# Performance work log

Measured on AMD Instinct MI355X. Metric: run time of the kernel, lower is better.

The kernel has to match this reference:

```python
import jax, jax.numpy as jnp
import numpy as np

TEMPERATURE = 0.2
EPS = 1e-12

def _l2norm(v, axis=-1):
    return v / jnp.maximum(jnp.linalg.norm(v, axis=axis, keepdims=True), EPS)

def setup_inputs() -> dict:
    key = jax.random.key(0)
    k1, k2, k3, k4, k5 = jax.random.split(key, 5)
    B, D, P, K = 4096, 256, 100, 10
    return {
        "x": jax.random.normal(k1, (B, D), dtype=jnp.float32),
        "x_aug": jax.random.normal(k2, (B, D), dtype=jnp.float32),
        "proto_w": jax.random.normal(k3, (P, D), dtype=jnp.float32),
        "hard_q": jax.random.randint(k4, (2, B), 0, P, dtype=jnp.int32),
        "neg_q": jax.random.randint(k5, (2, B, K), 0, P, dtype=jnp.int32),
    }

def reference(x, x_aug, proto_w, hard_q, neg_q):
    # graphcl.loss_cal with args.hard_selection=True, args.proto_dist=True,
    # args.sample_dist=False. The original O(n^2) python loops are vectorized
    # as gathers/broadcasts; math is identical.
    B = x.shape[0]
    P = proto_w.shape[0]
    out1 = _l2norm(x)                      # [B, D]
    out2 = _l2norm(x_aug)                  # [B, D]
    out = jnp.concatenate([out1, out2], 0) # [2B, D]
    n = 2 * B

    sim = jnp.exp(out @ out.T / TEMPERATURE)          # [2B, 2B]
    eye = jnp.eye(n, dtype=bool)

    hq = hard_q.reshape(-1)                # [2B]  (concat of the two views)
    nq = neg_q.reshape(n, -1)              # [2B, K]

    # hard_selection: mask[i,j] = (i != j) and (hard_q[j] in neg_q[i]).
    # Build per-prototype membership [2B, P], then gather columns by hq[j].
    mem_proto = (nq[:, :, None] == jnp.arange(P, dtype=nq.dtype)[None, None, :]).any(1)  # [2B, P]
    member = jnp.take(mem_proto, hq, axis=1)          # [2B, 2B]
    mask = (~eye) & member

    # proto_dist reweighting (prototypes used via .data, i.e. detached).
    w = _l2norm(jax.lax.stop_gradient(proto_w))       # [P, D]
    pd = 1.0 - w @ w.T                                # [P, P]
    rw = jnp.where(eye, 0.0, pd[hq[:, None], hq[None, :]])  # [2B, 2B]
    rmin = rw.min(axis=1, keepdims=True)
    rmax = rw.max(axis=1, keepdims=True)
    rw = (rw - rmin) / (rmax - rmin)
    # NOTE: torch broadcasts (2B,2B) - (2B,) along columns -> mu[None, :]
    mu = rw.mean(axis=1)
    std = jnp.std(rw, axis=1, ddof=1)  # torch.std default: unbiased
    rw = jnp.exp((rw - mu[None, :]) ** 2 / (2.0 * std[None, :] ** 2))
    sim = sim * rw

    pos = jnp.exp(jnp.sum(out1 * out2, axis=-1) / TEMPERATURE)  # [B]
    pos = jnp.concatenate([pos, pos], 0)                        # [2B]
    # masked_select(...).sum(dim=-1) in the original sums ALL kept entries.
    denom = jnp.sum(jnp.where(mask, sim, 0.0))
    loss = jnp.mean(-jnp.log(pos / denom))
    return loss
```

## Files before the change

### kernel.cpp

```cpp
#include <hip/hip_runtime.h>
#include <cmath>

#define BB   4096
#define DD   256
#define NN   8192
#define PP   100
#define KK   10

typedef float f32x16 __attribute__((ext_vector_type(16)));
typedef long  lx2    __attribute__((ext_vector_type(2)));

constexpr size_t OFF_DPART = 0;
constexpr size_t OFF_PPART = 4096;
constexpr size_t OFF_CNT   = 8192;
constexpr size_t OFF_MU    = 8704;
constexpr size_t OFF_SD    = 9216;
constexpr size_t OFF_RWN   = 9728;
constexpr size_t OFF_BASE  = 49728;
constexpr size_t OFF_PI    = 56128;
constexpr size_t OFF_INVP  = 88896;
constexpr size_t OFF_HQP   = 121664;
constexpr size_t OFF_CTABT = 154432;
constexpr size_t OFF_G     = 3431232;


__global__ __launch_bounds__(1024) void prep_kernel(
    const int* __restrict__ hq, int* __restrict__ cnt, int* __restrict__ base16,
    double* __restrict__ dpart, double* __restrict__ ppart) {
    __shared__ int h[16][PP];
    __shared__ int sc[PP];
    const int t = threadIdx.x;
    h[t & 15][t >> 4] = 0;
    if (t < 576) h[(t + 1024) & 15][(t + 1024) >> 4] = 0;
    if (t < 512) dpart[t] = 0.0; else ppart[t - 512] = 0.0;
    __syncthreads();
#pragma unroll
    for (int r = 0; r < 8; ++r) {
        const int i = r * 1024 + t;
        atomicAdd(&h[2 * r + (t >> 9)][hq[i]], 1);
    }
    __syncthreads();
    int bb[16];
    if (t < PP) {
        int s = 0;
#pragma unroll
        for (int ch = 0; ch < 16; ++ch) { bb[ch] = s; s += h[ch][t]; }
        cnt[t] = s;
        sc[t] = s;
    }
    __syncthreads();
    if (t == 0) {
        int run = 0;
        for (int c = 0; c < PP; ++c) { int v = sc[c]; sc[c] = run; run += v; }
    }
    __syncthreads();
    if (t < PP) {
        const int cb = sc[t];
#pragma unroll
        for (int ch = 0; ch < 16; ++ch) base16[ch * PP + t] = cb + bb[ch];
    }
}

__global__ __launch_bounds__(256) void scatter_kernel(
    const int* __restrict__ hq, const int* __restrict__ base16,
    int* __restrict__ pi, int* __restrict__ invp, int* __restrict__ hqp) {
    __shared__ int cur[PP];
    const int t = threadIdx.x;
    const int ch = blockIdx.x;
    if (t < PP) cur[t] = base16[ch * PP + t];
    __syncthreads();
#pragma unroll
    for (int r = 0; r < 2; ++r) {
        const int i = ch * 512 + r * 256 + t;
        const int c = hq[i];
        const int d = atomicAdd(&cur[c], 1);
        pi[d] = i;
        hqp[d] = c;
        invp[i] = d;
    }
}

__global__ __launch_bounds__(256) void norm_protopd_kernel(
    const float* __restrict__ x, const float* __restrict__ xa,
    const float* __restrict__ pw, const int* __restrict__ invp,
    const int* __restrict__ cnt, char* __restrict__ Gpb, double* __restrict__ ppart,
    float* __restrict__ rwn, float* __restrict__ mu, float* __restrict__ sd) {
    const int blk = blockIdx.x;
    const int t = threadIdx.x;
    if (blk < 1024) {
        const int wv = t >> 6, lane = t & 63;
        const int i = blk * 4 + wv;
        const float4 v1 = *(const float4*)(x  + (size_t)i * DD + lane * 4);
        const float4 v2 = *(const float4*)(xa + (size_t)i * DD + lane * 4);
        float a = v1.x * v1.x + v1.y * v1.y + v1.z * v1.z + v1.w * v1.w;
        float b = v2.x * v2.x + v2.y * v2.y + v2.z * v2.z + v2.w * v2.w;
        float c = v1.x * v2.x + v1.y * v2.y + v1.z * v2.z + v1.w * v2.w;
#pragma unroll
        for (int off = 32; off > 0; off >>= 1) {
            a += __shfl_xor(a, off);
            b += __shfl_xor(b, off);
            c += __shfl_xor(c, off);
        }
        const float d1 = fmaxf(sqrtf(a), 1e-12f), i1 = 1.0f / d1;
        const float d2 = fmaxf(sqrtf(b), 1e-12f), i2 = 1.0f / d2;
        const int p1 = invp[i];
        const int p2 = invp[i + BB];
        int w1 = __builtin_amdgcn_cvt_pk_fp8_f32(v1.x * i1, v1.y * i1, 0, false);
        w1 = __builtin_amdgcn_cvt_pk_fp8_f32(v1.z * i1, v1.w * i1, w1, true);
        int w2 = __builtin_amdgcn_cvt_pk_fp8_f32(v2.x * i2, v2.y * i2, 0, false);
        w2 = __builtin_amdgcn_cvt_pk_fp8_f32(v2.z * i2, v2.w * i2, w2, true);
        const int q = lane >> 3, halfsel = (lane >> 1) & 1, pairsel = (lane >> 2) & 1;
        const int bo = pairsel * 8 + 4 * (lane & 1);
        const size_t a1 = (size_t)((p1 >> 5) * 8192 + q * 1024 +
                                   (halfsel * 32 + (p1 & 31)) * 16 + bo);
        const size_t a2 = (size_t)((p2 >> 5) * 8192 + q * 1024 +
                                   (halfsel * 32 + (p2 & 31)) * 16 + bo);
        *(int*)(Gpb + a1) = w1;
        *(int*)(Gpb + a2) = w2;
        if (lane == 0) atomicAdd(&ppart[i & 511], (double)(c * i1 * i2));
    } else {
        const int a = blk - 1024;
        __shared__ alignas(16) float wa[DD];
        __shared__ float pdrow[PP];
        __shared__ float r4[4];
        float av = pw[(size_t)a * DD + t];
        float ss = av * av;
#pragma unroll
        for (int off = 32; off > 0; off >>= 1) ss += __shfl_down(ss, off);
        if ((t & 63) == 0) r4[t >> 6] = ss;
        __syncthreads();
        const float na = fmaxf(sqrtf(r4[0] + r4[1] + r4[2] + r4[3]), 1e-12f);
        wa[t] = av / na;
        __syncthreads();
        if (t < PP) {
            const float4* wc = (const float4*)(pw + (size_t)t * DD);
            float dot = 0.f, nb = 0.f;
#pragma unroll 4
            for (int k = 0; k < 64; ++k) {
                const float4 w = wc[k];
                const float4 u = *(const float4*)(wa + 4 * k);
                dot += u.x * w.x + u.y * w.y + u.z * w.z + u.w * w.w;
                nb += w.x * w.x + w.y * w.y + w.z * w.z + w.w * w.w;
            }
            pdrow[t] = 1.0f - dot / fmaxf(sqrtf(nb), 1e-12f);
        }
        __syncthreads();
        if (t < 64) {
            const int lane = t;
            float vmin = 0.f, vmax = 0.f;
            for (int b = lane; b < PP; b += 64) {
                int cc = cnt[b] - (b == a ? 1 : 0);
                if (cc > 0) {
                    float v = pdrow[b];
                    vmin = fminf(vmin, v);
                    vmax = fmaxf(vmax, v);
                }
            }
#pragma unroll
            for (int off = 32; off > 0; off >>= 1) {
                vmin = fminf(vmin, __shfl_xor(vmin, off));
                vmax = fmaxf(vmax, __shfl_xor(vmax, off));
            }
            const float den = vmax - vmin;
            const float inv = (den > 0.f) ? 1.f / den : 0.f;
            double s1 = 0.0, s2 = 0.0;
            for (int b = lane; b < PP; b += 64) {
                float v = (pdrow[b] - vmin) * inv;
                rwn[a * PP + b] = v;
                int cc = cnt[b] - (b == a ? 1 : 0);
                if (cc > 0) { double dv = v; s1 += cc * dv; s2 += cc * dv * dv; }
            }
            if (lane == 0) { double v0 = (0.0 - (double)vmin) * inv; s1 += v0; s2 += v0 * v0; }
#pragma unroll
            for (int off = 32; off > 0; off >>= 1) {
                s1 += __shfl_xor(s1, off);
                s2 += __shfl_xor(s2, off);
            }
            if (lane == 0) {
                double m = s1 / (double)NN;
                double var = (s2 - (double)NN * m * m) / (double)(NN - 1);
                mu[a] = (float)m;
                sd[a] = (float)sqrt(fmax(var, 0.0));
            }
        }
    }
}

__global__ __launch_bounds__(256) void ctab_kernel(
    const int* __restrict__ pi, const int* __restrict__ hqp, const int* __restrict__ nq,
    const float* __restrict__ rwn, const float* __restrict__ mu, const float* __restrict__ sd,
    float* __restrict__ CtabT) {
    const int p0 = blockIdx.x * 32;
    const int t = threadIdx.x;
    __shared__ unsigned long long bits[32][2];
    __shared__ int cls[32];
    __shared__ float smu[PP], ssd[PP];
    if (t < 32) {
        const int p = p0 + t;
        const int* row = nq + (size_t)pi[p] * KK;
        unsigned long long b0 = 0, b1 = 0;
#pragma unroll
        for (int k = 0; k < KK; ++k) {
            int c = row[k];
            if (c < 64) b0 |= 1ull << c; else b1 |= 1ull << (c - 64);
        }
        bits[t][0] = b0;
        bits[t][1] = b1;
        cls[t] = hqp[p];
    }
    if (t < PP) { smu[t] = mu[t]; ssd[t] = sd[t]; }
    __syncthreads();
    for (int idx = t; idx < 32 * PP; idx += 256) {
        const int c = idx >> 5;
        const int pl = idx & 31;
        const bool m = (c < 64) ? ((bits[pl][0] >> c) & 1) : ((bits[pl][1] >> (c - 64)) & 1);
        float v = 0.f;
        if (m) {
            float d = rwn[cls[pl] * PP + c] - smu[c];
            float s = ssd[c];
            v = expf(d * d / (2.0f * s * s));
        }
        CtabT[(size_t)c * NN + p0 + pl] = v;
    }
}

__device__ __forceinline__ void gload_lds16(void* g, void* l) {
    typedef __attribute__((address_space(1))) void* as1_void_p;
    typedef __attribute__((address_space(3))) void* as3_void_p;
    __builtin_amdgcn_global_load_lds((as1_void_p)g, (as3_void_p)l, 16, 0, 0);
}

__global__ __launch_bounds__(256) void sim_kernel(
    const char* __restrict__ Gpb, const int* __restrict__ hqp,
    const float* __restrict__ CtabT, double* __restrict__ dpart) {
    const int xcd = blockIdx.x & 7;
    int idx0 = blockIdx.x >> 3;
    if (idx0 >= 496 + (xcd >> 1) * 16) return;
    int idx = idx0;
    int bj = 0, bi = 0;
#pragma unroll
    for (int q = 0; q < 16; ++q) {
        const int bjq = xcd + 8 * q;
        const int c = (bjq >> 1) + 1;
        if (idx < c) { bj = bjq; bi = idx; break; }
        idx -= c;
    }

    const int t = threadIdx.x;
    const int lane = t & 63;
    const int wv = t >> 6;
    const int i0w = bi * 128 + wv * 32;
    const int j0 = bj * 64;

    __shared__ alignas(16) char lB[16384];

    const char* pa = Gpb + (size_t)(i0w >> 5) * 8192 + lane * 16;
    lx2 a[8];
#pragma unroll
    for (int q = 0; q < 8; ++q) a[q] = *(const lx2*)(pa + q * 1024);

    char* gB = const_cast<char*>(Gpb) + (size_t)(j0 >> 5) * 8192;
#pragma unroll
    for (int s = 0; s < 4; ++s) {
        const int off = (s * 4 + wv) * 1024;
        gload_lds16(gB + off + lane * 16, lB + off);
    }

    const int cl = lane & 31, h = lane >> 5;
    const int col0 = j0 + cl;
    const int col1 = j0 + 32 + cl;
    const int cls0 = hqp[col0];
    const int cls1 = hqp[col1];
    int4 rcg[4];
#pragma unroll
    for (int g = 0; g < 4; ++g)
        rcg[g] = *(const int4*)(hqp + i0w + 8 * g + 4 * h);

    __syncthreads();

    f32x16 acc[2] = {};
#pragma unroll
    for (int q = 0; q < 8; ++q) {
        const lx2 b0 = *(const lx2*)(lB + q * 1024 + lane * 16);
        const lx2 b1 = *(const lx2*)(lB + 8192 + q * 1024 + lane * 16);
        acc[0] = __builtin_amdgcn_mfma_f32_32x32x16_fp8_fp8(a[q].x, b0.x, acc[0], 0, 0, 0);
        acc[1] = __builtin_amdgcn_mfma_f32_32x32x16_fp8_fp8(a[q].x, b1.x, acc[1], 0, 0, 0);
        acc[0] = __builtin_amdgcn_mfma_f32_32x32x16_fp8_fp8(a[q].y, b0.y, acc[0], 0, 0, 0);
        acc[1] = __builtin_amdgcn_mfma_f32_32x32x16_fp8_fp8(a[q].y, b1.y, acc[1], 0, 0, 0);
    }

    const float* ct0 = CtabT + (size_t)cls0 * NN;
    const float* ct1 = CtabT + (size_t)cls1 * NN;
    float partial = 0.f;
#pragma unroll
    for (int g = 0; g < 4; ++g) {
        const int rbase = i0w + 8 * g + 4 * h;
        const float4 cf0 = *(const float4*)(ct0 + rbase);
        const float4 cf1 = *(const float4*)(ct1 + rbase);
        const float* f0 = (const float*)&cf0;
        const float* f1 = (const float*)&cf1;
        const int rcv[4] = {rcg[g].x, rcg[g].y, rcg[g].z, rcg[g].w};
#pragma unroll
        for (int r = 0; r < 4; ++r) {
            const int row = rbase + r;
            const float* ctr = CtabT + (size_t)rcv[r] * NN;
            const float c20 = ctr[col0];
            const float c21 = ctr[col1];
            const float e0 = __expf(acc[0][4 * g + r] * 5.0f);
            const float e1 = __expf(acc[1][4 * g + r] * 5.0f);
            partial += (row < col0) ? e0 * (f0[r] + c20) : 0.f;
            partial += (row < col1) ? e1 * (f1[r] + c21) : 0.f;
        }
    }
#pragma unroll
    for (int off = 32; off > 0; off >>= 1) partial += __shfl_down(partial, off);
    __shared__ float wsum[4];
    if (lane == 0) wsum[wv] = partial;
    __syncthreads();
    if (t == 0) {
        const int slot = (xcd * 8 + (idx0 & 7)) * 8 + ((idx0 >> 3) & 7);
        atomicAdd(&dpart[slot], (double)(wsum[0] + wsum[1] + wsum[2] + wsum[3]));
    }
}

__global__ void finalize_kernel(const double* __restrict__ dpart,
                                const double* __restrict__ ppart, float* __restrict__ out) {
    const int lane = threadIdx.x;
    double d = 0.0, p = 0.0;
#pragma unroll
    for (int k = 0; k < 8; ++k) {
        d += dpart[lane + 64 * k];
        p += ppart[lane + 64 * k];
    }
#pragma unroll
    for (int off = 32; off > 0; off >>= 1) {
        d += __shfl_down(d, off);
        p += __shfl_down(p, off);
    }
    if (lane == 0) out[0] = (float)(log(d) - p * (5.0 / 4096.0));
}

extern "C" void kernel_launch(void* const* d_in, const int* in_sizes, int n_in,
                              void* d_out, int out_size, void* d_ws, size_t ws_size,
                              hipStream_t stream) {
    const float* x  = (const float*)d_in[0];
    const float* xa = (const float*)d_in[1];
    const float* pw = (const float*)d_in[2];
    const int* hq   = (const int*)d_in[3];
    const int* nq   = (const int*)d_in[4];
    float* out      = (float*)d_out;

    char* ws = (char*)d_ws;
    double* dpart = (double*)(ws + OFF_DPART);
    double* ppart = (double*)(ws + OFF_PPART);
    int* cnt      = (int*)(ws + OFF_CNT);
    float* mu     = (float*)(ws + OFF_MU);
    float* sd     = (float*)(ws + OFF_SD);
    float* rwn    = (float*)(ws + OFF_RWN);
    int* base16   = (int*)(ws + OFF_BASE);
    int* pi       = (int*)(ws + OFF_PI);
    int* invp     = (int*)(ws + OFF_INVP);
    int* hqp      = (int*)(ws + OFF_HQP);
    float* CtabT  = (float*)(ws + OFF_CTABT);
    char* Gpb     = (char*)(ws + OFF_G);

    prep_kernel<<<1, 1024, 0, stream>>>(hq, cnt, base16, dpart, ppart);
    scatter_kernel<<<16, 256, 0, stream>>>(hq, base16, pi, invp, hqp);
    norm_protopd_kernel<<<1124, 256, 0, stream>>>(x, xa, pw, invp, cnt, Gpb, ppart,
                                                  rwn, mu, sd);
    ctab_kernel<<<NN / 32, 256, 0, stream>>>(pi, hqp, nq, rwn, mu, sd, CtabT);
    sim_kernel<<<8 * 544, 256, 0, stream>>>(Gpb, hqp, CtabT, dpart);
    finalize_kernel<<<1, 64, 0, stream>>>(dpart, ppart, out);
}
```

Measured before the change: 125.9 us.

## Merge prep and scatter kernels, batch norm rows per wave, hoist Ctab loads

Folds the single-block histogram/prefix kernel and the 16-block scatter kernel into one 17-block kernel. Each block recomputes the full histogram redundantly to get its own scatter bases, and an extra block zeroes the accumulators and writes the class counts. The normalization kernel now handles four rows per wave with loads issued up front, which cuts its block count and the number of ppart atomics. In the sim kernel, all Ctab gathers are issued before the exp/accumulate loop to overlap their latency. The cost is redundant histogram work per block and higher register pressure.

```diff
diff --git a/kernel.cpp b/kernel.cpp
--- a/kernel.cpp
+++ b/kernel.cpp
@@ -16,7 +16,6 @@
 constexpr size_t OFF_MU    = 8704;
 constexpr size_t OFF_SD    = 9216;
 constexpr size_t OFF_RWN   = 9728;
-constexpr size_t OFF_BASE  = 49728;
 constexpr size_t OFF_PI    = 56128;
 constexpr size_t OFF_INVP  = 88896;
 constexpr size_t OFF_HQP   = 121664;
@@ -24,56 +23,59 @@
 constexpr size_t OFF_G     = 3431232;
 
 
-__global__ __launch_bounds__(1024) void prep_kernel(
-    const int* __restrict__ hq, int* __restrict__ cnt, int* __restrict__ base16,
+__global__ __launch_bounds__(256) void sortzero_kernel(
+    const int* __restrict__ hq, int* __restrict__ cnt,
+    int* __restrict__ pi, int* __restrict__ invp, int* __restrict__ hqp,
     double* __restrict__ dpart, double* __restrict__ ppart) {
+    const int blk = blockIdx.x;
+    const int t = threadIdx.x;
+    if (blk == 16) {
+        for (int k = t; k < 512; k += 256) { dpart[k] = 0.0; ppart[k] = 0.0; }
+        __shared__ int hh[PP];
+        if (t < PP) hh[t] = 0;
+        __syncthreads();
+#pragma unroll
+        for (int r = 0; r < 32; ++r) atomicAdd(&hh[hq[r * 256 + t]], 1);
+        __syncthreads();
+        if (t < PP) cnt[t] = hh[t];
+        return;
+    }
     __shared__ int h[16][PP];
-    __shared__ int sc[PP];
-    const int t = threadIdx.x;
-    h[t & 15][t >> 4] = 0;
-    if (t < 576) h[(t + 1024) & 15][(t + 1024) >> 4] = 0;
-    if (t < 512) dpart[t] = 0.0; else ppart[t - 512] = 0.0;
-    __syncthreads();
-#pragma unroll
-    for (int r = 0; r < 8; ++r) {
-        const int i = r * 1024 + t;
-        atomicAdd(&h[2 * r + (t >> 9)][hq[i]], 1);
-    }
-    __syncthreads();
-    int bb[16];
+    __shared__ int tot[PP];
+    __shared__ int gbase[PP];
+    __shared__ int base[PP];
+    int* hf = &h[0][0];
+    for (int k = t; k < 16 * PP; k += 256) hf[k] = 0;
+    __syncthreads();
+#pragma unroll
+    for (int r = 0; r < 32; ++r) {
+        const int i = r * 256 + t;
+        atomicAdd(&h[r >> 1][hq[i]], 1);
+    }
+    __syncthreads();
     if (t < PP) {
-        int s = 0;
-#pragma unroll
-        for (int ch = 0; ch < 16; ++ch) { bb[ch] = s; s += h[ch][t]; }
-        cnt[t] = s;
-        sc[t] = s;
+        int pre = 0, s = 0;
+#pragma unroll
+        for (int ch = 0; ch < 16; ++ch) {
+            if (ch == blk) pre = s;
+            s += h[ch][t];
+        }
+        tot[t] = s;
+        base[t] = pre;
     }
     __syncthreads();
     if (t == 0) {
         int run = 0;
-        for (int c = 0; c < PP; ++c) { int v = sc[c]; sc[c] = run; run += v; }
-    }
-    __syncthreads();
-    if (t < PP) {
-        const int cb = sc[t];
-#pragma unroll
-        for (int ch = 0; ch < 16; ++ch) base16[ch * PP + t] = cb + bb[ch];
-    }
-}
-
-__global__ __launch_bounds__(256) void scatter_kernel(
-    const int* __restrict__ hq, const int* __restrict__ base16,
-    int* __restrict__ pi, int* __restrict__ invp, int* __restrict__ hqp) {
-    __shared__ int cur[PP];
-    const int t = threadIdx.x;
-    const int ch = blockIdx.x;
-    if (t < PP) cur[t] = base16[ch * PP + t];
+        for (int c = 0; c < PP; ++c) { gbase[c] = run; run += tot[c]; }
+    }
+    __syncthreads();
+    if (t < PP) base[t] += gbase[t];
     __syncthreads();
 #pragma unroll
     for (int r = 0; r < 2; ++r) {
-        const int i = ch * 512 + r * 256 + t;
+        const int i = blk * 512 + r * 256 + t;
         const int c = hq[i];
-        const int d = atomicAdd(&cur[c], 1);
+        const int d = atomicAdd(&base[c], 1);
         pi[d] = i;
         hqp[d] = c;
         invp[i] = d;
@@ -87,39 +89,50 @@
     float* __restrict__ rwn, float* __restrict__ mu, float* __restrict__ sd) {
     const int blk = blockIdx.x;
     const int t = threadIdx.x;
-    if (blk < 1024) {
+    if (blk < 256) {
         const int wv = t >> 6, lane = t & 63;
-        const int i = blk * 4 + wv;
-        const float4 v1 = *(const float4*)(x  + (size_t)i * DD + lane * 4);
-        const float4 v2 = *(const float4*)(xa + (size_t)i * DD + lane * 4);
-        float a = v1.x * v1.x + v1.y * v1.y + v1.z * v1.z + v1.w * v1.w;
-        float b = v2.x * v2.x + v2.y * v2.y + v2.z * v2.z + v2.w * v2.w;
-        float c = v1.x * v2.x + v1.y * v2.y + v1.z * v2.z + v1.w * v2.w;
-#pragma unroll
-        for (int off = 32; off > 0; off >>= 1) {
-            a += __shfl_xor(a, off);
-            b += __shfl_xor(b, off);
-            c += __shfl_xor(c, off);
-        }
-        const float d1 = fmaxf(sqrtf(a), 1e-12f), i1 = 1.0f / d1;
-        const float d2 = fmaxf(sqrtf(b), 1e-12f), i2 = 1.0f / d2;
-        const int p1 = invp[i];
-        const int p2 = invp[i + BB];
-        int w1 = __builtin_amdgcn_cvt_pk_fp8_f32(v1.x * i1, v1.y * i1, 0, false);
-        w1 = __builtin_amdgcn_cvt_pk_fp8_f32(v1.z * i1, v1.w * i1, w1, true);
-        int w2 = __builtin_amdgcn_cvt_pk_fp8_f32(v2.x * i2, v2.y * i2, 0, false);
-        w2 = __builtin_amdgcn_cvt_pk_fp8_f32(v2.z * i2, v2.w * i2, w2, true);
+        const int w = blk * 4 + wv;
+        float4 v1[4], v2[4];
+        int p1[4], p2[4];
+#pragma unroll
+        for (int s = 0; s < 4; ++s) {
+            const int i = w + 1024 * s;
+            v1[s] = *(const float4*)(x  + (size_t)i * DD + lane * 4);
+            v2[s] = *(const float4*)(xa + (size_t)i * DD + lane * 4);
+            p1[s] = invp[i];
+            p2[s] = invp[i + BB];
+        }
         const int q = lane >> 3, halfsel = (lane >> 1) & 1, pairsel = (lane >> 2) & 1;
         const int bo = pairsel * 8 + 4 * (lane & 1);
-        const size_t a1 = (size_t)((p1 >> 5) * 8192 + q * 1024 +
-                                   (halfsel * 32 + (p1 & 31)) * 16 + bo);
-        const size_t a2 = (size_t)((p2 >> 5) * 8192 + q * 1024 +
-                                   (halfsel * 32 + (p2 & 31)) * 16 + bo);
-        *(int*)(Gpb + a1) = w1;
-        *(int*)(Gpb + a2) = w2;
-        if (lane == 0) atomicAdd(&ppart[i & 511], (double)(c * i1 * i2));
+        double psum = 0.0;
+#pragma unroll
+        for (int s = 0; s < 4; ++s) {
+            float a = v1[s].x * v1[s].x + v1[s].y * v1[s].y + v1[s].z * v1[s].z + v1[s].w * v1[s].w;
+            float b = v2[s].x * v2[s].x + v2[s].y * v2[s].y + v2[s].z * v2[s].z + v2[s].w * v2[s].w;
+            float c = v1[s].x * v2[s].x + v1[s].y * v2[s].y + v1[s].z * v2[s].z + v1[s].w * v2[s].w;
+#pragma unroll
+            for (int off = 32; off > 0; off >>= 1) {
+                a += __shfl_xor(a, off);
+                b += __shfl_xor(b, off);
+                c += __shfl_xor(c, off);
+            }
+            const float d1 = fmaxf(sqrtf(a), 1e-12f), i1 = 1.0f / d1;
+            const float d2 = fmaxf(sqrtf(b), 1e-12f), i2 = 1.0f / d2;
+            int w1 = __builtin_amdgcn_cvt_pk_fp8_f32(v1[s].x * i1, v1[s].y * i1, 0, false);
+            w1 = __builtin_amdgcn_cvt_pk_fp8_f32(v1[s].z * i1, v1[s].w * i1, w1, true);
+            int w2 = __builtin_amdgcn_cvt_pk_fp8_f32(v2[s].x * i2, v2[s].y * i2, 0, false);
+            w2 = __builtin_amdgcn_cvt_pk_fp8_f32(v2[s].z * i2, v2[s].w * i2, w2, true);
+            const size_t a1 = (size_t)((p1[s] >> 5) * 8192 + q * 1024 +
+                                       (halfsel * 32 + (p1[s] & 31)) * 16 + bo);
+            const size_t a2 = (size_t)((p2[s] >> 5) * 8192 + q * 1024 +
+                                       (halfsel * 32 + (p2[s] & 31)) * 16 + bo);
+            *(int*)(Gpb + a1) = w1;
+            *(int*)(Gpb + a2) = w2;
+            psum += (double)(c * i1 * i2);
+        }
+        if (lane == 0) atomicAdd(&ppart[w & 511], psum);
     } else {
-        const int a = blk - 1024;
+        const int a = blk - 256;
         __shared__ alignas(16) float wa[DD];
         __shared__ float pdrow[PP];
         __shared__ float r4[4];
@@ -291,25 +304,34 @@
 
     const float* ct0 = CtabT + (size_t)cls0 * NN;
     const float* ct1 = CtabT + (size_t)cls1 * NN;
-    float partial = 0.f;
+    float4 cf0[4], cf1[4];
+    float c20[4][4], c21[4][4];
 #pragma unroll
     for (int g = 0; g < 4; ++g) {
         const int rbase = i0w + 8 * g + 4 * h;
-        const float4 cf0 = *(const float4*)(ct0 + rbase);
-        const float4 cf1 = *(const float4*)(ct1 + rbase);
-        const float* f0 = (const float*)&cf0;
-        const float* f1 = (const float*)&cf1;
+        cf0[g] = *(const float4*)(ct0 + rbase);
+        cf1[g] = *(const float4*)(ct1 + rbase);
         const int rcv[4] = {rcg[g].x, rcg[g].y, rcg[g].z, rcg[g].w};
+#pragma unroll
+        for (int r = 0; r < 4; ++r) {
+            const float* ctr = CtabT + (size_t)rcv[r] * NN;
+            c20[g][r] = ctr[col0];
+            c21[g][r] = ctr[col1];
+        }
+    }
+    float partial = 0.f;
+#pragma unroll
+    for (int g = 0; g < 4; ++g) {
+        const int rbase = i0w + 8 * g + 4 * h;
+        const float* f0 = (const float*)&cf0[g];
+        const float* f1 = (const float*)&cf1[g];
 #pragma unroll
         for (int r = 0; r < 4; ++r) {
             const int row = rbase + r;
-            const float* ctr = CtabT + (size_t)rcv[r] * NN;
-            const float c20 = ctr[col0];
-            const float c21 = ctr[col1];
             const float e0 = __expf(acc[0][4 * g + r] * 5.0f);
             const float e1 = __expf(acc[1][4 * g + r] * 5.0f);
-            partial += (row < col0) ? e0 * (f0[r] + c20) : 0.f;
-            partial += (row < col1) ? e1 * (f1[r] + c21) : 0.f;
+            partial += (row < col0) ? e0 * (f0[r] + c20[g][r]) : 0.f;
+            partial += (row < col1) ? e1 * (f1[r] + c21[g][r]) : 0.f;
         }
     }
 #pragma unroll
@@ -357,17 +379,15 @@
     float* mu     = (float*)(ws + OFF_MU);
     float* sd     = (float*)(ws + OFF_SD);
     float* rwn    = (float*)(ws + OFF_RWN);
-    int* base16   = (int*)(ws + OFF_BASE);
     int* pi       = (int*)(ws + OFF_PI);
     int* invp     = (int*)(ws + OFF_INVP);
     int* hqp      = (int*)(ws + OFF_HQP);
     float* CtabT  = (float*)(ws + OFF_CTABT);
     char* Gpb     = (char*)(ws + OFF_G);
 
-    prep_kernel<<<1, 1024, 0, stream>>>(hq, cnt, base16, dpart, ppart);
-    scatter_kernel<<<16, 256, 0, stream>>>(hq, base16, pi, invp, hqp);
-    norm_protopd_kernel<<<1124, 256, 0, stream>>>(x, xa, pw, invp, cnt, Gpb, ppart,
-                                                  rwn, mu, sd);
+    sortzero_kernel<<<17, 256, 0, stream>>>(hq, cnt, pi, invp, hqp, dpart, ppart);
+    norm_protopd_kernel<<<356, 256, 0, stream>>>(x, xa, pw, invp, cnt, Gpb, ppart,
+                                                 rwn, mu, sd);
     ctab_kernel<<<NN / 32, 256, 0, stream>>>(pi, hqp, nq, rwn, mu, sd, CtabT);
     sim_kernel<<<8 * 544, 256, 0, stream>>>(Gpb, hqp, CtabT, dpart);
     finalize_kernel<<<1, 64, 0, stream>>>(dpart, ppart, out);
```

New measurement: 123.4 us. -2.0%, faster.
